# Performance work log

Measured on AMD Instinct MI355X. Metric: run time of the kernel, lower is better.

The kernel has to match this reference:

```python
import jax, jax.numpy as jnp
import numpy as np

DIM, NUM_HEADS, WINDOW = 1024, 16, 256
HEAD_DIM = DIM // NUM_HEADS
B, L = 2, 2048


def rotate_half(x):
    x1, x2 = jnp.split(x, 2, axis=-1)
    return jnp.concatenate([-x2, x1], axis=-1)


def setup_inputs() -> dict:
    key = jax.random.key(0)
    kx, kq, kk, kv, ko = jax.random.split(key, 5)
    x = jax.random.normal(kx, (B, L, DIM), dtype=jnp.float32)
    # realistic RoPE tables (L, head_dim)
    inv_freq = 1.0 / (10000.0 ** (np.arange(0, HEAD_DIM, 2, dtype=np.float32) / HEAD_DIM))
    ang = np.arange(L, dtype=np.float32)[:, None] * inv_freq[None, :]  # (L, hd/2)
    ang = np.concatenate([ang, ang], axis=-1)  # (L, hd)
    cos = jnp.asarray(np.cos(ang))
    sin = jnp.asarray(np.sin(ang))
    scale = 1.0 / np.sqrt(DIM)
    Wq = jax.random.normal(kq, (DIM, DIM), dtype=jnp.float32) * scale
    Wk = jax.random.normal(kk, (DIM, DIM), dtype=jnp.float32) * scale
    Wv = jax.random.normal(kv, (DIM, DIM), dtype=jnp.float32) * scale
    Wo = jax.random.normal(ko, (DIM, DIM), dtype=jnp.float32) * scale
    return {"x": x, "cos": cos, "sin": sin, "Wq": Wq, "Wk": Wk, "Wv": Wv, "Wo": Wo}


def reference(x, cos, sin, Wq, Wk, Wv, Wo):
    Bx, Lx, D = x.shape
    H, hd, w = NUM_HEADS, HEAD_DIM, WINDOW
    q = (x @ Wq.T).reshape(Bx, Lx, H, hd)
    k = (x @ Wk.T).reshape(Bx, Lx, H, hd)
    v = (x @ Wv.T).reshape(Bx, Lx, H, hd)
    c = cos[None, :, None, :]  # broadcast over batch, heads
    s = sin[None, :, None, :]
    q = q * c + rotate_half(q) * s
    k = k * c + rotate_half(k) * s
    # (B, H, L, hd)
    q = q.transpose(0, 2, 1, 3)
    k = k.transpose(0, 2, 1, 3)
    v = v.transpose(0, 2, 1, 3)
    i = jnp.arange(Lx)[:, None]
    j = jnp.arange(Lx)[None, :]
    # causal & within sliding window: i - w <= j <= i
    mask = (j <= i) & (j >= i - w)
    scores = jnp.einsum("bhqd,bhkd->bhqk", q, k) / jnp.sqrt(jnp.asarray(hd, x.dtype))
    scores = jnp.where(mask[None, None], scores, jnp.finfo(scores.dtype).min)
    attn = jax.nn.softmax(scores, axis=-1)
    out = jnp.einsum("bhqk,bhkd->bhqd", attn, v)
    out = out.transpose(0, 2, 1, 3).reshape(Bx, Lx, D)
    return out @ Wo.T
```

## Files before the change

### kernel.cpp

```cpp
#include <hip/hip_runtime.h>

#define DIM 1024
#define NH  16
#define HD  64
#define BB  2
#define LL  2048
#define WIN 256
#define MM  (BB * LL)
#define NQKV (3 * DIM)
#define SEG  (DIM * DIM)

typedef __bf16 bf16x8 __attribute__((ext_vector_type(8)));
typedef float  f32x4  __attribute__((ext_vector_type(4)));
typedef unsigned short u16x8 __attribute__((ext_vector_type(8)));

__device__ __forceinline__ unsigned short f2bf(float f) {
    union { float f; unsigned int i; } v; v.f = f;
    unsigned int r = v.i + 0x7fffu + ((v.i >> 16) & 1u);
    return (unsigned short)(r >> 16);
}
__device__ __forceinline__ bf16x8 load8bf(const unsigned short* p) {
    uint4 u = *reinterpret_cast<const uint4*>(p);
    return __builtin_bit_cast(bf16x8, u);
}
__device__ __forceinline__ void gll16(const void* g, void* l) {
    __builtin_amdgcn_global_load_lds(
        (const __attribute__((address_space(1))) unsigned int*)g,
        (__attribute__((address_space(3))) unsigned int*)l, 16, 0, 0);
}

__global__ __launch_bounds__(256) void convert_inputs(
    const float* __restrict__ x,
    const float* __restrict__ Wq, const float* __restrict__ Wk,
    const float* __restrict__ Wv, const float* __restrict__ Wo,
    unsigned short* __restrict__ xb,
    unsigned short* __restrict__ wqkv,
    unsigned short* __restrict__ wob)
{
    const int y = blockIdx.y;
    const size_t base = ((size_t)blockIdx.x * 256 + threadIdx.x) * 8;
    const float* src; unsigned short* dst;
    if (y < 4)       { src = x + (size_t)y * SEG;  dst = xb + (size_t)y * SEG; }
    else if (y == 4) { src = Wq; dst = wqkv; }
    else if (y == 5) { src = Wk; dst = wqkv + SEG; }
    else if (y == 6) { src = Wv; dst = wqkv + 2 * (size_t)SEG; }
    else             { src = Wo; dst = wob; }
    float4 a = ((const float4*)(src + base))[0];
    float4 b = ((const float4*)(src + base))[1];
    u16x8 r;
    r[0] = f2bf(a.x); r[1] = f2bf(a.y); r[2] = f2bf(a.z); r[3] = f2bf(a.w);
    r[4] = f2bf(b.x); r[5] = f2bf(b.y); r[6] = f2bf(b.z); r[7] = f2bf(b.w);
    *(u16x8*)(dst + base) = r;
}

__global__ __launch_bounds__(256, 4) void qkv_gemm(
    const unsigned short* __restrict__ xb,
    const unsigned short* __restrict__ wqkv,
    const float* __restrict__ cosb, const float* __restrict__ sinb,
    unsigned short* __restrict__ qws, unsigned short* __restrict__ kws,
    unsigned short* __restrict__ vT)
{
    __shared__ __align__(16) unsigned short smem[2 * 128 * 64];
    unsigned short* As = smem;
    unsigned short* Bs = smem + 128 * 64;
    const int t = threadIdx.x;
    const int lane = t & 63, w = t >> 6;
    const int wm = w >> 1, wn = w & 1;
    const int lr = lane & 15, quad = lane >> 4;

    const int id   = blockIdx.y * 24 + blockIdx.x;
    const int xcd  = id & 7, slot = id >> 3;
    const int bxn  = (xcd & 1) * 12 + (slot % 12);
    const int byn  = (xcd >> 1) * 8 + (slot / 12);
    const int n0 = bxn * 128, m0 = byn * 128;

    f32x4 acc[4][4];
    for (int i = 0; i < 4; i++) for (int j = 0; j < 4; j++) acc[i][j] = 0.0f;

    const int rsub = t >> 3;
    const int csw  = (t & 7) ^ (rsub & 7);
    const int sw7  = lr & 7;

    for (int k0 = 0; k0 < DIM; k0 += 64) {
        __syncthreads();
        #pragma unroll
        for (int p = 0; p < 4; p++) {
            const int row = p * 32 + rsub;
            gll16(xb   + (size_t)(m0 + row) * DIM + k0 + csw * 8,
                  &As[p * 2048 + t * 8]);
            gll16(wqkv + (size_t)(n0 + row) * DIM + k0 + csw * 8,
                  &Bs[p * 2048 + t * 8]);
        }
        __syncthreads();
        #pragma unroll
        for (int kk = 0; kk < 2; kk++) {
            bf16x8 af[4], bfr[4];
            #pragma unroll
            for (int mi = 0; mi < 4; mi++) {
                const int R = wm * 64 + mi * 16 + lr;
                af[mi] = load8bf(&As[R * 64 + (((kk * 4 + quad) ^ sw7) * 8)]);
            }
            #pragma unroll
            for (int ni = 0; ni < 4; ni++) {
                const int R = wn * 64 + ni * 16 + lr;
                bfr[ni] = load8bf(&Bs[R * 64 + (((kk * 4 + quad) ^ sw7) * 8)]);
            }
            #pragma unroll
            for (int mi = 0; mi < 4; mi++)
                #pragma unroll
                for (int ni = 0; ni < 4; ni++)
                    acc[mi][ni] = __builtin_amdgcn_mfma_f32_16x16x32_bf16(
                        af[mi], bfr[ni], acc[mi][ni], 0, 0, 0);
        }
    }

    const int ng = n0 + wn * 64;
    const int which = ng >> 10;
    const int h = (ng & (DIM - 1)) >> 6;

    if (which == 2) {
        __syncthreads();
        unsigned short* T = smem + w * 2048;
        const int token0 = m0 + wm * 64;
        const int b  = token0 >> 11;
        const int lg = (token0 & (LL - 1)) + (lane & 7) * 8;
        #pragma unroll
        for (int p = 0; p < 2; p++) {
            #pragma unroll
            for (int ni = 2 * p; ni < 2 * p + 2; ni++) {
                const int dl = (ni & 1) * 16 + lr;
                const int g4 = (dl & 7) << 2;
                #pragma unroll
                for (int mi = 0; mi < 4; mi++)
                    #pragma unroll
                    for (int reg = 0; reg < 4; reg++) {
                        const int l = mi * 16 + quad * 4 + reg;
                        const int cw = (l >> 1) ^ g4;
                        T[dl * 64 + cw * 2 + (l & 1)] = f2bf(acc[mi][ni][reg]);
                    }
            }
            #pragma unroll
            for (int s = 0; s < 4; s++) {
                const int dl = s * 8 + (lane >> 3);
                const int d  = p * 32 + dl;
                const int g4 = (dl & 7) << 2;
                const int pd = ((lane & 7) * 4) ^ g4;
                uint4 val = *(const uint4*)&T[dl * 64 + pd * 2];
                *(uint4*)&vT[((size_t)(b * NH + h) * HD + d) * LL + lg] = val;
            }
        }
    } else {
        unsigned short* dst = (which == 0) ? qws : kws;
        #pragma unroll
        for (int mi = 0; mi < 4; mi++) {
            #pragma unroll
            for (int reg = 0; reg < 4; reg++) {
                const int row = m0 + wm * 64 + mi * 16 + quad * 4 + reg;
                const int b = row >> 11, l = row & (LL - 1);
                #pragma unroll
                for (int ni = 0; ni < 4; ni++) {
                    const int d = ni * 16 + lr;
                    const float c = cosb[l * HD + d];
                    const float s = sinb[l * HD + d];
                    const float partner = (d < 32) ? -acc[mi][ni + 2][reg]
                                                   :  acc[mi][ni - 2][reg];
                    dst[((size_t)(b * NH + h) * LL + l) * HD + d] =
                        f2bf(acc[mi][ni][reg] * c + partner * s);
                }
            }
        }
    }
}

#define SW_SPAN 320
#define PSTR 40
__global__ __launch_bounds__(256, 3) void swa_attn(
    const unsigned short* __restrict__ qws,
    const unsigned short* __restrict__ kws,
    const unsigned short* __restrict__ vT,
    unsigned short* __restrict__ aout)
{
    __shared__ __align__(16) unsigned short Ks[SW_SPAN * 64];
    __shared__ __align__(16) unsigned short Pc[4][16][PSTR];

    const int t = threadIdx.x;
    const int lane = t & 63, w = t >> 6;

    const int id   = (blockIdx.z * 16 + blockIdx.y) * 32 + blockIdx.x;
    const int xcd  = id & 7, slot = id >> 3;
    const int hb   = xcd * 4 + (slot >> 5);
    const int qb   = slot & 31;
    const int h = hb & 15, b = hb >> 4;

    const int q0 = qb * 64;
    const int base_key = q0 - WIN;

    const int lr = lane & 15, quad = lane >> 4, ko = quad * 8;
    const size_t base = ((size_t)(b * NH + h)) * LL * HD;
    const unsigned short* Q  = qws + base;
    const unsigned short* K  = kws + base;
    const unsigned short* VT = vT + base;

    {
        const int rsub = t >> 3;
        const int csw  = (t & 7) ^ (rsub & 7);
        #pragma unroll
        for (int p = 0; p < 10; p++) {
            const int j = min(max(base_key + p * 32 + rsub, 0), LL - 1);
            gll16(K + (size_t)j * HD + csw * 8, &Ks[p * 2048 + t * 8]);
        }
    }
    const int i0 = q0 + w * 16;
    const int wkey = i0 - WIN;
    const bf16x8 qa0 = load8bf(Q + (size_t)(i0 + lr) * HD + ko);
    const bf16x8 qa1 = load8bf(Q + (size_t)(i0 + lr) * HD + 32 + ko);
    __syncthreads();

    float rowsum[4] = {0.f, 0.f, 0.f, 0.f};
    f32x4 o[4];
    #pragma unroll
    for (int nt = 0; nt < 4; nt++) o[nt] = 0.0f;

    if (q0 >= WIN) {
        bool mlo[4], mhi[4];
        #pragma unroll
        for (int reg = 0; reg < 4; reg++) {
            mlo[reg] = (lr >= quad * 4 + reg);
            mhi[reg] = (lr <= quad * 4 + reg);
        }
        bf16x8 bv[4];
        #pragma unroll
        for (int nt = 0; nt < 4; nt++)
            bv[nt] = load8bf(VT + (size_t)(nt * 16 + lr) * LL + wkey + ko);

        #pragma unroll
        for (int kc = 0; kc < 9; kc++) {
            #pragma unroll
            for (int sub = 0; sub < 2; sub++) {
                const int kt = 2 * kc + sub;
                if (kt > 16) {
                    #pragma unroll
                    for (int reg = 0; reg < 4; reg++)
                        Pc[w][quad * 4 + reg][16 + lr] = 0;
                } else {
                    const int R = w * 16 + kt * 16 + lr;
                    const bf16x8 kb0 = load8bf(&Ks[R * 64 + ((quad       ^ (R & 7)) * 8)]);
                    const bf16x8 kb1 = load8bf(&Ks[R * 64 + (((quad + 4) ^ (R & 7)) * 8)]);
                    f32x4 s = 0.0f;
                    s = __builtin_amdgcn_mfma_f32_16x16x32_bf16(qa0, kb0, s, 0, 0, 0);
                    s = __builtin_amdgcn_mfma_f32_16x16x32_bf16(qa1, kb1, s, 0, 0, 0);
                    #pragma unroll
                    for (int reg = 0; reg < 4; reg++) {
                        float e = __expf(s[reg] * 0.125f);
                        if (kt == 0)  e = mlo[reg] ? e : 0.0f;
                        if (kt == 16) e = mhi[reg] ? e : 0.0f;
                        rowsum[reg] += e;
                        Pc[w][quad * 4 + reg][sub * 16 + lr] = f2bf(e);
                    }
                }
            }
            bf16x8 bvn[4];
            if (kc < 8) {
                int kb = wkey + (kc + 1) * 32 + ko;
                kb = min(kb, LL - 8);
                #pragma unroll
                for (int nt = 0; nt < 4; nt++)
                    bvn[nt] = load8bf(VT + (size_t)(nt * 16 + lr) * LL + kb);
            }
            const bf16x8 pa = load8bf(&Pc[w][lr][ko]);
            #pragma unroll
            for (int nt = 0; nt < 4; nt++)
                o[nt] = __builtin_amdgcn_mfma_f32_16x16x32_bf16(pa, bv[nt], o[nt], 0, 0, 0);
            if (kc < 8) {
                #pragma unroll
                for (int nt = 0; nt < 4; nt++) bv[nt] = bvn[nt];
            }
        }
    } else {
        #pragma unroll
        for (int kc = 0; kc < 9; kc++) {
            #pragma unroll
            for (int sub = 0; sub < 2; sub++) {
                const int kt = 2 * kc + sub;
                const int R = min(w * 16 + kt * 16 + lr, SW_SPAN - 1);
                const bf16x8 kb0 = load8bf(&Ks[R * 64 + ((quad       ^ (R & 7)) * 8)]);
                const bf16x8 kb1 = load8bf(&Ks[R * 64 + (((quad + 4) ^ (R & 7)) * 8)]);
                f32x4 s = 0.0f;
                s = __builtin_amdgcn_mfma_f32_16x16x32_bf16(qa0, kb0, s, 0, 0, 0);
                s = __builtin_amdgcn_mfma_f32_16x16x32_bf16(qa1, kb1, s, 0, 0, 0);
                #pragma unroll
                for (int reg = 0; reg < 4; reg++) {
                    const int i = i0 + quad * 4 + reg;
                    const int j = wkey + kt * 16 + lr;
                    const bool valid = (j >= 0) && (j <= i) && (j >= i - WIN);
                    const float e = valid ? __expf(s[reg] * 0.125f) : 0.0f;
                    rowsum[reg] += e;
                    Pc[w][quad * 4 + reg][sub * 16 + lr] = f2bf(e);
                }
            }
            const bf16x8 pa = load8bf(&Pc[w][lr][ko]);
            int kb = wkey + kc * 32 + ko;
            kb = min(max(kb, 0), LL - 8);
            bf16x8 bv[4];
            #pragma unroll
            for (int nt = 0; nt < 4; nt++)
                bv[nt] = load8bf(VT + (size_t)(nt * 16 + lr) * LL + kb);
            #pragma unroll
            for (int nt = 0; nt < 4; nt++)
                o[nt] = __builtin_amdgcn_mfma_f32_16x16x32_bf16(pa, bv[nt], o[nt], 0, 0, 0);
        }
    }

    float inv[4];
    #pragma unroll
    for (int reg = 0; reg < 4; reg++) {
        float s = rowsum[reg];
        s += __shfl_xor(s, 1); s += __shfl_xor(s, 2);
        s += __shfl_xor(s, 4); s += __shfl_xor(s, 8);
        inv[reg] = 1.0f / s;
    }

    #pragma unroll
    for (int nt = 0; nt < 4; nt++) {
        #pragma unroll
        for (int reg = 0; reg < 4; reg++) {
            const int i = i0 + quad * 4 + reg;
            const int d = nt * 16 + lr;
            aout[((size_t)(b * LL + i)) * DIM + h * HD + d] =
                f2bf(o[nt][reg] * inv[reg]);
        }
    }
}

__global__ __launch_bounds__(256, 4) void out_gemm(
    const unsigned short* __restrict__ A,
    const unsigned short* __restrict__ Wob,
    float* __restrict__ out)
{
    __shared__ __align__(16) unsigned short smem[64 * 64 + 64 * 64];
    unsigned short* As = smem;
    unsigned short* Bs = smem + 64 * 64;
    const int t = threadIdx.x;
    const int lane = t & 63, w = t >> 6;
    const int wm = w >> 1, wn = w & 1;
    const int lr = lane & 15, quad = lane >> 4;

    const int id   = blockIdx.y * 16 + blockIdx.x;
    const int xcd  = id & 7, slot = id >> 3;
    const int bx   = (xcd & 1) * 8 + (slot & 7);
    const int by   = (xcd >> 1) * 16 + (slot >> 3);
    const int n0 = bx * 64, m0 = by * 64;

    f32x4 acc[2][2];
    for (int i = 0; i < 2; i++) for (int j = 0; j < 2; j++) acc[i][j] = 0.0f;

    const int rsub = t >> 3;
    const int csw  = (t & 7) ^ (rsub & 7);
    const int sw7  = lr & 7;

    for (int k0 = 0; k0 < DIM; k0 += 64) {
        __syncthreads();
        #pragma unroll
        for (int p = 0; p < 2; p++) {
            const int row = p * 32 + rsub;
            gll16(A   + (size_t)(m0 + row) * DIM + k0 + csw * 8,
                  &As[p * 2048 + t * 8]);
            gll16(Wob + (size_t)(n0 + row) * DIM + k0 + csw * 8,
                  &Bs[p * 2048 + t * 8]);
        }
        __syncthreads();
        #pragma unroll
        for (int kk = 0; kk < 2; kk++) {
            bf16x8 af[2], bfr[2];
            #pragma unroll
            for (int mi = 0; mi < 2; mi++) {
                const int R = wm * 32 + mi * 16 + lr;
                af[mi] = load8bf(&As[R * 64 + (((kk * 4 + quad) ^ sw7) * 8)]);
            }
            #pragma unroll
            for (int ni = 0; ni < 2; ni++) {
                const int R = wn * 32 + ni * 16 + lr;
                bfr[ni] = load8bf(&Bs[R * 64 + (((kk * 4 + quad) ^ sw7) * 8)]);
            }
            #pragma unroll
            for (int mi = 0; mi < 2; mi++)
                #pragma unroll
                for (int ni = 0; ni < 2; ni++)
                    acc[mi][ni] = __builtin_amdgcn_mfma_f32_16x16x32_bf16(
                        af[mi], bfr[ni], acc[mi][ni], 0, 0, 0);
        }
    }

    #pragma unroll
    for (int mi = 0; mi < 2; mi++) {
        #pragma unroll
        for (int reg = 0; reg < 4; reg++) {
            const int row = m0 + wm * 32 + mi * 16 + quad * 4 + reg;
            #pragma unroll
            for (int ni = 0; ni < 2; ni++) {
                const int col = n0 + wn * 32 + ni * 16 + lr;
                out[(size_t)row * DIM + col] = acc[mi][ni][reg];
            }
        }
    }
}

extern "C" void kernel_launch(void* const* d_in, const int* in_sizes, int n_in,
                              void* d_out, int out_size, void* d_ws, size_t ws_size,
                              hipStream_t stream)
{
    const float* x    = (const float*)d_in[0];
    const float* cosb = (const float*)d_in[1];
    const float* sinb = (const float*)d_in[2];
    const float* Wq   = (const float*)d_in[3];
    const float* Wk   = (const float*)d_in[4];
    const float* Wv   = (const float*)d_in[5];
    const float* Wo   = (const float*)d_in[6];
    float* out = (float*)d_out;

    unsigned short* xb   = (unsigned short*)d_ws;
    unsigned short* wqkv = xb + (size_t)MM * DIM;
    unsigned short* wob  = wqkv + (size_t)NQKV * DIM;
    unsigned short* qws  = wob + (size_t)DIM * DIM;
    unsigned short* kws  = qws + (size_t)BB * NH * LL * HD;
    unsigned short* vT   = kws + (size_t)BB * NH * LL * HD;
    unsigned short* aws  = xb;

    convert_inputs<<<dim3(SEG / (256 * 8), 8), 256, 0, stream>>>(
        x, Wq, Wk, Wv, Wo, xb, wqkv, wob);
    qkv_gemm<<<dim3(NQKV / 128, MM / 128), 256, 0, stream>>>(
        xb, wqkv, cosb, sinb, qws, kws, vT);
    swa_attn<<<dim3(LL / 64, NH, BB), 256, 0, stream>>>(qws, kws, vT, aws);
    out_gemm<<<dim3(DIM / 64, MM / 64), 256, 0, stream>>>(aws, wob, out);
}
```

Baseline: 158.2 us.

## Load K directly from global memory in attention, dropping shared K staging

New measurement: 165.0 us. 4.3% more time.

```diff
diff --git a/kernel.cpp b/kernel.cpp
--- a/kernel.cpp
+++ b/kernel.cpp
@@ -172,15 +172,13 @@
     }
 }
 
-#define SW_SPAN 320
 #define PSTR 40
-__global__ __launch_bounds__(256, 3) void swa_attn(
+__global__ __launch_bounds__(256, 4) void swa_attn(
     const unsigned short* __restrict__ qws,
     const unsigned short* __restrict__ kws,
     const unsigned short* __restrict__ vT,
     unsigned short* __restrict__ aout)
 {
-    __shared__ __align__(16) unsigned short Ks[SW_SPAN * 64];
     __shared__ __align__(16) unsigned short Pc[4][16][PSTR];
 
     const int t = threadIdx.x;
@@ -193,7 +191,6 @@
     const int h = hb & 15, b = hb >> 4;
 
     const int q0 = qb * 64;
-    const int base_key = q0 - WIN;
 
     const int lr = lane & 15, quad = lane >> 4, ko = quad * 8;
     const size_t base = ((size_t)(b * NH + h)) * LL * HD;
@@ -201,20 +198,10 @@
     const unsigned short* K  = kws + base;
     const unsigned short* VT = vT + base;
 
-    {
-        const int rsub = t >> 3;
-        const int csw  = (t & 7) ^ (rsub & 7);
-        #pragma unroll
-        for (int p = 0; p < 10; p++) {
-            const int j = min(max(base_key + p * 32 + rsub, 0), LL - 1);
-            gll16(K + (size_t)j * HD + csw * 8, &Ks[p * 2048 + t * 8]);
-        }
-    }
     const int i0 = q0 + w * 16;
     const int wkey = i0 - WIN;
     const bf16x8 qa0 = load8bf(Q + (size_t)(i0 + lr) * HD + ko);
     const bf16x8 qa1 = load8bf(Q + (size_t)(i0 + lr) * HD + 32 + ko);
-    __syncthreads();
 
     float rowsum[4] = {0.f, 0.f, 0.f, 0.f};
     f32x4 o[4];
@@ -228,53 +215,58 @@
             mlo[reg] = (lr >= quad * 4 + reg);
             mhi[reg] = (lr <= quad * 4 + reg);
         }
-        bf16x8 bv[4];
-        #pragma unroll
-        for (int nt = 0; nt < 4; nt++)
-            bv[nt] = load8bf(VT + (size_t)(nt * 16 + lr) * LL + wkey + ko);
-
         #pragma unroll
         for (int kc = 0; kc < 9; kc++) {
-            #pragma unroll
-            for (int sub = 0; sub < 2; sub++) {
-                const int kt = 2 * kc + sub;
+            {
+                const int kt = 2 * kc;
+                const int jr = wkey + kt * 16 + lr;
+                const bf16x8 kb0 = load8bf(K + (size_t)jr * HD + ko);
+                const bf16x8 kb1 = load8bf(K + (size_t)jr * HD + 32 + ko);
+                f32x4 s = 0.0f;
+                s = __builtin_amdgcn_mfma_f32_16x16x32_bf16(qa0, kb0, s, 0, 0, 0);
+                s = __builtin_amdgcn_mfma_f32_16x16x32_bf16(qa1, kb1, s, 0, 0, 0);
+                #pragma unroll
+                for (int reg = 0; reg < 4; reg++) {
+                    float e = __expf(s[reg] * 0.125f);
+                    if (kt == 0)  e = mlo[reg] ? e : 0.0f;
+                    if (kt == 16) e = mhi[reg] ? e : 0.0f;
+                    rowsum[reg] += e;
+                    Pc[w][quad * 4 + reg][lr] = f2bf(e);
+                }
+            }
+            bf16x8 bv[4];
+            {
+                int kb = wkey + kc * 32 + ko;
+                kb = min(kb, LL - 8);
+                #pragma unroll
+                for (int nt = 0; nt < 4; nt++)
+                    bv[nt] = load8bf(VT + (size_t)(nt * 16 + lr) * LL + kb);
+            }
+            {
+                const int kt = 2 * kc + 1;
                 if (kt > 16) {
                     #pragma unroll
                     for (int reg = 0; reg < 4; reg++)
                         Pc[w][quad * 4 + reg][16 + lr] = 0;
                 } else {
-                    const int R = w * 16 + kt * 16 + lr;
-                    const bf16x8 kb0 = load8bf(&Ks[R * 64 + ((quad       ^ (R & 7)) * 8)]);
-                    const bf16x8 kb1 = load8bf(&Ks[R * 64 + (((quad + 4) ^ (R & 7)) * 8)]);
+                    const int jr = wkey + kt * 16 + lr;
+                    const bf16x8 kb0 = load8bf(K + (size_t)jr * HD + ko);
+                    const bf16x8 kb1 = load8bf(K + (size_t)jr * HD + 32 + ko);
                     f32x4 s = 0.0f;
                     s = __builtin_amdgcn_mfma_f32_16x16x32_bf16(qa0, kb0, s, 0, 0, 0);
                     s = __builtin_amdgcn_mfma_f32_16x16x32_bf16(qa1, kb1, s, 0, 0, 0);
                     #pragma unroll
                     for (int reg = 0; reg < 4; reg++) {
-                        float e = __expf(s[reg] * 0.125f);
-                        if (kt == 0)  e = mlo[reg] ? e : 0.0f;
-                        if (kt == 16) e = mhi[reg] ? e : 0.0f;
+                        const float e = __expf(s[reg] * 0.125f);
                         rowsum[reg] += e;
-                        Pc[w][quad * 4 + reg][sub * 16 + lr] = f2bf(e);
+                        Pc[w][quad * 4 + reg][16 + lr] = f2bf(e);
                     }
                 }
             }
-            bf16x8 bvn[4];
-            if (kc < 8) {
-                int kb = wkey + (kc + 1) * 32 + ko;
-                kb = min(kb, LL - 8);
-                #pragma unroll
-                for (int nt = 0; nt < 4; nt++)
-                    bvn[nt] = load8bf(VT + (size_t)(nt * 16 + lr) * LL + kb);
-            }
             const bf16x8 pa = load8bf(&Pc[w][lr][ko]);
             #pragma unroll
             for (int nt = 0; nt < 4; nt++)
                 o[nt] = __builtin_amdgcn_mfma_f32_16x16x32_bf16(pa, bv[nt], o[nt], 0, 0, 0);
-            if (kc < 8) {
-                #pragma unroll
-                for (int nt = 0; nt < 4; nt++) bv[nt] = bvn[nt];
-            }
         }
     } else {
         #pragma unroll
@@ -282,16 +274,16 @@
             #pragma unroll
             for (int sub = 0; sub < 2; sub++) {
                 const int kt = 2 * kc + sub;
-                const int R = min(w * 16 + kt * 16 + lr, SW_SPAN - 1);
-                const bf16x8 kb0 = load8bf(&Ks[R * 64 + ((quad       ^ (R & 7)) * 8)]);
-                const bf16x8 kb1 = load8bf(&Ks[R * 64 + (((quad + 4) ^ (R & 7)) * 8)]);
+                const int j  = wkey + kt * 16 + lr;
+                const int jc = min(max(j, 0), LL - 1);
+                const bf16x8 kb0 = load8bf(K + (size_t)jc * HD + ko);
+                const bf16x8 kb1 = load8bf(K + (size_t)jc * HD + 32 + ko);
                 f32x4 s = 0.0f;
                 s = __builtin_amdgcn_mfma_f32_16x16x32_bf16(qa0, kb0, s, 0, 0, 0);
                 s = __builtin_amdgcn_mfma_f32_16x16x32_bf16(qa1, kb1, s, 0, 0, 0);
                 #pragma unroll
                 for (int reg = 0; reg < 4; reg++) {
                     const int i = i0 + quad * 4 + reg;
-                    const int j = wkey + kt * 16 + lr;
                     const bool valid = (j >= 0) && (j <= i) && (j >= i - WIN);
                     const float e = valid ? __expf(s[reg] * 0.125f) : 0.0f;
                     rowsum[reg] += e;
```
